# Kernel optimization log

Measured on AMD Instinct MI355X. Metric: run time of the kernel, lower is better.

Reference implementation:

```python
import jax, jax.numpy as jnp
import numpy as np

B, D, K, C, A = 131072, 300, 32, 384, 18  # batch, emb dim, num_negs, codebook size, attr dims


def setup_inputs() -> dict:
    key = jax.random.key(0)
    ks = jax.random.split(key, 12)
    x = jax.random.normal(ks[0], (B, D), dtype=jnp.float32)
    # codebook of all possible attribute one-hot combinations (binary rows)
    codebook = (jax.random.uniform(ks[1], (C, A)) < 0.5).astype(jnp.float32)
    tgt = jax.random.randint(ks[2], (B,), 0, C)
    y = codebook[tgt]                                   # true labels are codebook rows
    ob = (jax.random.uniform(ks[3], (B, A)) > 0.1).astype(jnp.float32)  # observed-attr mask
    neg_idx = jax.random.randint(ks[4], (B, K), 0, C)   # negative sample indices
    s = 0.05
    W1 = jax.random.normal(ks[5], (D, 64), dtype=jnp.float32) * s
    b1 = jnp.zeros((64,), jnp.float32)
    W2 = jax.random.normal(ks[6], (64, 32), dtype=jnp.float32) * s
    b2 = jnp.zeros((32,), jnp.float32)
    W3 = jax.random.normal(ks[7], (32, A), dtype=jnp.float32) * s
    b3 = jnp.zeros((A,), jnp.float32)
    return dict(x=x, y=y, ob=ob, codebook=codebook, W1=W1, b1=b1, W2=W2, b2=b2,
                W3=W3, b3=b3, neg_idx=neg_idx)


def reference(x, y, ob, codebook, W1, b1, W2, b2, W3, b3, neg_idx):
    # MLP: Linear->Sigmoid->Linear->Sigmoid->Linear
    h = jax.nn.sigmoid(x @ W1 + b1)
    h = jax.nn.sigmoid(h @ W2 + b2)
    W_user = h @ W3 + b3                                # [B, A]
    W_compact = W_user * ob                             # [B, A]
    # rows kept by the original index_select: nonzero row-sum -> mask instead
    mask = (jnp.sum(W_compact, axis=1) != 0).astype(W_compact.dtype)  # [B]
    neg = codebook[neg_idx]                             # [B, K, A] gather
    # neg log term: sum over negatives and attr dims of log sigmoid(-(neg * w))
    neg_log = jax.nn.log_sigmoid(-neg * W_compact[:, None, :]).sum(axis=(1, 2))  # [B]
    pos_log = jax.nn.log_sigmoid(W_compact * y).sum(axis=1)                      # [B]
    cnt = jnp.maximum(jnp.sum(mask), 1.0)
    loss = -jnp.sum(mask * (pos_log + neg_log)) / cnt
    return W_user, loss
```

## Files before the change

### kernel.cpp

```cpp
#include <hip/hip_runtime.h>

typedef short bf16x8 __attribute__((ext_vector_type(8)));
typedef unsigned short u16;
typedef u16 u16x4 __attribute__((ext_vector_type(4)));
typedef float f32x4 __attribute__((ext_vector_type(4)));

constexpr int TPB  = 256;
constexpr int RPB  = 64;
constexpr int DIM  = 300;
constexpr int KPAD = 320;
constexpr int NKT  = 10;
constexpr int H1N  = 64;
constexpr int H2N  = 32;
constexpr int NA   = 18;
constexpr int NK   = 32;
constexpr int NC   = 384;
constexpr float LOG_HALF = -0.6931471805599453f;

__device__ __forceinline__ float fast_sigmoid(float z) {
    return __builtin_amdgcn_rcpf(1.0f + __expf(-z));
}
__device__ __forceinline__ float lsig(float z) {
    return fminf(z, 0.0f) - __logf(1.0f + __expf(-fabsf(z)));
}
__device__ __forceinline__ u16 f2bf(float f) {
    unsigned u = __builtin_bit_cast(unsigned, f);
    return (u16)((u + 0x7FFFu + ((u >> 16) & 1u)) >> 16);
}
__device__ __forceinline__ unsigned spread8(unsigned v) {
    v = (v | (v << 12)) & 0x000F000Fu;
    v = (v | (v << 6))  & 0x03030303u;
    v = (v | (v << 3))  & 0x11111111u;
    return v;
}

__global__ __launch_bounds__(384)
void prep_k(const float* __restrict__ W1, const float* __restrict__ W2,
            const float* __restrict__ W3, const float* __restrict__ cbf,
            u16* __restrict__ w1t, u16* __restrict__ w2t, u16* __restrict__ w3t,
            unsigned* __restrict__ cbw)
{
    const int c = blockIdx.x;
    const int t = threadIdx.x;
    if (c < 64) {
        if (t < KPAD)
            w1t[c * KPAD + t] = f2bf((t < DIM) ? W1[t * H1N + c] : 0.0f);
    } else if (c == 64) {
        if (t < NC) {
            unsigned bits = 0u;
            #pragma unroll
            for (int a = 0; a < NA; ++a)
                bits |= (cbf[t * NA + a] != 0.0f) ? (1u << a) : 0u;
            cbw[t] = bits;
        }
    } else if (c == 65) {
        for (int e = t; e < H2N * H1N; e += 384) {
            const int n = e >> 6, k = e & 63;
            w2t[e] = f2bf(W2[k * H2N + n]);
        }
    } else {
        for (int e = t; e < H2N * H2N; e += 384) {
            const int n = e >> 5, k = e & 31;
            w3t[e] = f2bf((n < NA) ? W3[k * NA + n] : 0.0f);
        }
    }
}

__global__ __launch_bounds__(TPB, 4)
void fused_mf2(const float* __restrict__ x, const float* __restrict__ y,
               const float* __restrict__ ob, const float* __restrict__ b1,
               const float* __restrict__ b2, const float* __restrict__ b3,
               const int* __restrict__ neg_idx,
               const u16* __restrict__ w1t, const u16* __restrict__ w2t,
               const u16* __restrict__ w3t, const unsigned* __restrict__ cbw,
               float* __restrict__ out_wu, float2* __restrict__ blk_part)
{
    __shared__ __align__(16) unsigned char smem[40960];
    u16*      xs      = (u16*)smem;
    u16*      h1s     = (u16*)smem;
    u16*      h2s     = (u16*)(smem + 8192);
    float*    wus     = (float*)(smem + 12288);
    unsigned* cb_bits = (unsigned*)(smem + 17408);
    float*    wsum    = (float*)(smem + 18944);
    int*      wcnt    = (int*)(smem + 18960);

    const int tid  = threadIdx.x;
    const int lane = tid & 63;
    const int wv   = tid >> 6;
    const int l15  = lane & 15;
    const int kg   = (lane >> 4) * 8;
    const long brow = (long)blockIdx.x * RPB;
    const float* xg = x + brow * DIM;

    float4 va[7], vb[6], vc[6];
    #pragma unroll
    for (int ch = 0; ch < 7; ++ch)
        va[ch] = *(const float4*)(xg + (long)(ch * TPB + tid) * 4);
    #pragma unroll
    for (int ch = 0; ch < 6; ++ch)
        vb[ch] = *(const float4*)(xg + (long)((7 + ch) * TPB + tid) * 4);
    __builtin_amdgcn_sched_barrier(0);
    #pragma unroll
    for (int ch = 0; ch < 7; ++ch) {
        const int f = ch * TPB + tid;
        const int row = f / 75, k = (f - row * 75) * 4;
        const int kk = k ^ ((row & 7) << 3);
        u16x4 pk = { f2bf(va[ch].x), f2bf(va[ch].y), f2bf(va[ch].z), f2bf(va[ch].w) };
        *(u16x4*)(xs + row * KPAD + kk) = pk;
    }
    __builtin_amdgcn_sched_barrier(0);
    #pragma unroll
    for (int ch = 0; ch < 6; ++ch) {
        const int f = (13 + ch) * TPB + tid;
        vc[ch] = (ch < 5 || f < 4800) ? *(const float4*)(xg + (long)f * 4)
                                      : make_float4(0.f, 0.f, 0.f, 0.f);
    }
    __builtin_amdgcn_sched_barrier(0);
    #pragma unroll
    for (int ch = 0; ch < 6; ++ch) {
        const int f = (7 + ch) * TPB + tid;
        const int row = f / 75, k = (f - row * 75) * 4;
        const int kk = k ^ ((row & 7) << 3);
        u16x4 pk = { f2bf(vb[ch].x), f2bf(vb[ch].y), f2bf(vb[ch].z), f2bf(vb[ch].w) };
        *(u16x4*)(xs + row * KPAD + kk) = pk;
    }
    #pragma unroll
    for (int ch = 0; ch < 6; ++ch) {
        const int f = (13 + ch) * TPB + tid;
        if (ch < 5 || f < 4800) {
            const int row = f / 75, k = (f - row * 75) * 4;
            const int kk = k ^ ((row & 7) << 3);
            u16x4 pk = { f2bf(vc[ch].x), f2bf(vc[ch].y), f2bf(vc[ch].z), f2bf(vc[ch].w) };
            *(u16x4*)(xs + row * KPAD + kk) = pk;
        }
    }
    #pragma unroll
    for (int uu = 0; uu < 5; ++uu) {
        const int e = uu * TPB + tid;
        const int row = e / 20, kp = e - row * 20;
        xs[row * KPAD + ((DIM + kp) ^ ((row & 7) << 3))] = 0;
    }

    const int colB = wv * 16 + l15;
    bf16x8 bfr[NKT];
    #pragma unroll
    for (int kt = 0; kt < NKT; ++kt)
        bfr[kt] = *(const bf16x8*)(w1t + colB * KPAD + kt * 32 + kg);
    const unsigned cbv0 = cbw[tid];
    const unsigned cbv1 = (tid < NC - TPB) ? cbw[tid + TPB] : 0u;

    __syncthreads();

    f32x4 acc[4];
    #pragma unroll
    for (int rt = 0; rt < 4; ++rt) acc[rt] = (f32x4){0.f, 0.f, 0.f, 0.f};
    #pragma unroll
    for (int kt = 0; kt < NKT; ++kt) {
        bf16x8 afr[4];
        #pragma unroll
        for (int rt = 0; rt < 4; ++rt) {
            const int row = rt * 16 + l15;
            afr[rt] = *(const bf16x8*)(xs + ((row * KPAD + kt * 32 + kg) ^ ((row & 7) << 3)));
        }
        #pragma unroll
        for (int rt = 0; rt < 4; ++rt)
            acc[rt] = __builtin_amdgcn_mfma_f32_16x16x32_bf16(afr[rt], bfr[kt], acc[rt], 0, 0, 0);
    }
    __syncthreads();

    const float b1v = b1[colB];
    #pragma unroll
    for (int rt = 0; rt < 4; ++rt) {
        #pragma unroll
        for (int j = 0; j < 4; ++j) {
            const int row = rt * 16 + (lane >> 4) * 4 + j;
            h1s[(row * H1N + colB) ^ ((row & 7) << 3)] = f2bf(fast_sigmoid(acc[rt][j] + b1v));
        }
    }
    cb_bits[tid] = cbv0;
    if (tid < NC - TPB) cb_bits[tid + TPB] = cbv1;

    const int rloc = wv * 16 + (lane >> 2);
    const int p    = lane & 3;
    const long bds = brow + rloc;
    const int4* nbp = (const int4*)(neg_idx + bds * NK + p * 8);
    const int4 n0 = nbp[0], n1 = nbp[1];
    const float* obr = ob + bds * NA + p * 4;
    const float2 oA = *(const float2*)obr, oB = *(const float2*)(obr + 2);
    const float  oT = (p < 2) ? ob[bds * NA + 16 + p] : 0.f;
    const float* yr = y + bds * NA + p * 4;
    const float2 yA = *(const float2*)yr, yB = *(const float2*)(yr + 2);
    const float  yT = (p < 2) ? y[bds * NA + 16 + p] : 0.f;

    __syncthreads();

    const int rowA = wv * 16 + l15;
    bf16x8 a2[2];
    #pragma unroll
    for (int kt = 0; kt < 2; ++kt)
        a2[kt] = *(const bf16x8*)(h1s + ((rowA * H1N + kt * 32 + kg) ^ ((rowA & 7) << 3)));
    f32x4 acc2[2];
    #pragma unroll
    for (int ct = 0; ct < 2; ++ct) {
        const float bb = b2[ct * 16 + l15];
        acc2[ct] = (f32x4){bb, bb, bb, bb};
    }
    #pragma unroll
    for (int ct = 0; ct < 2; ++ct)
        #pragma unroll
        for (int kt = 0; kt < 2; ++kt) {
            const bf16x8 bfr2 = *(const bf16x8*)(w2t + (ct * 16 + l15) * H1N + kt * 32 + kg);
            acc2[ct] = __builtin_amdgcn_mfma_f32_16x16x32_bf16(a2[kt], bfr2, acc2[ct], 0, 0, 0);
        }
    #pragma unroll
    for (int ct = 0; ct < 2; ++ct) {
        #pragma unroll
        for (int j = 0; j < 4; ++j) {
            const int row = wv * 16 + (lane >> 4) * 4 + j;
            const int col = ct * 16 + l15;
            h2s[(row * H2N + col) ^ ((row & 3) << 3)] = f2bf(fast_sigmoid(acc2[ct][j]));
        }
    }

    const bf16x8 a3 = *(const bf16x8*)(h2s + ((rowA * H2N + kg) ^ ((rowA & 3) << 3)));
    f32x4 acc3[2];
    #pragma unroll
    for (int ct = 0; ct < 2; ++ct) {
        const int col = ct * 16 + l15;
        const float bb = (col < NA) ? b3[col] : 0.f;
        acc3[ct] = (f32x4){bb, bb, bb, bb};
    }
    #pragma unroll
    for (int ct = 0; ct < 2; ++ct) {
        const bf16x8 bfr3 = *(const bf16x8*)(w3t + (ct * 16 + l15) * H2N + kg);
        acc3[ct] = __builtin_amdgcn_mfma_f32_16x16x32_bf16(a3, bfr3, acc3[ct], 0, 0, 0);
    }
    #pragma unroll
    for (int j = 0; j < 4; ++j) {
        const int row = wv * 16 + (lane >> 4) * 4 + j;
        wus[row * 20 + l15] = acc3[0][j];
        if (l15 < 2) wus[row * 20 + 16 + l15] = acc3[1][j];
    }
    __builtin_amdgcn_sched_barrier(0);

    const float4 wA = *(const float4*)(wus + rloc * 20 + p * 4);
    const float  wT = (p < 2) ? wus[rloc * 20 + 16 + p] : 0.f;

    const float wcv[4] = {wA.x * oA.x, wA.y * oA.y, wA.z * oB.x, wA.w * oB.y};
    const float yvv[4] = {yA.x, yA.y, yB.x, yB.y};
    const float wcT = wT * oT;
    float ssum = wcv[0] + wcv[1] + wcv[2] + wcv[3] + wcT;
    ssum += __shfl_xor(ssum, 1);
    ssum += __shfl_xor(ssum, 2);
    const int mask = (ssum != 0.0f) ? 1 : 0;

    const int ids[8] = {n0.x, n0.y, n0.z, n0.w, n1.x, n1.y, n1.z, n1.w};
    unsigned c0 = 0u, c1 = 0u, c2 = 0u;
    #pragma unroll
    for (int kk = 0; kk < 8; ++kk) {
        const unsigned bits = cb_bits[ids[kk]];
        c0 += spread8(bits & 0xFFu);
        c1 += spread8((bits >> 8) & 0xFFu);
        const unsigned t = (bits >> 16) & 3u;
        c2 += (t | (t << 3)) & 0x11u;
    }
    unsigned e0 = c0 & 0x0F0F0F0Fu;
    unsigned e1 = (c0 >> 4) & 0x0F0F0F0Fu;
    unsigned e2 = c1 & 0x0F0F0F0Fu;
    unsigned e3 = (c1 >> 4) & 0x0F0F0F0Fu;
    unsigned e4 = (c2 & 15u) | (((c2 >> 4) & 15u) << 8);
    e0 += __shfl_xor((int)e0, 1); e0 += __shfl_xor((int)e0, 2);
    e1 += __shfl_xor((int)e1, 1); e1 += __shfl_xor((int)e1, 2);
    e2 += __shfl_xor((int)e2, 1); e2 += __shfl_xor((int)e2, 2);
    e3 += __shfl_xor((int)e3, 1); e3 += __shfl_xor((int)e3, 2);
    e4 += __shfl_xor((int)e4, 1); e4 += __shfl_xor((int)e4, 2);

    float rsum = 0.0f;
    #pragma unroll
    for (int i = 0; i < 4; ++i) {
        const unsigned regE = ((i & 1) == 0) ? ((p < 2) ? e0 : e2)
                                             : ((p < 2) ? e1 : e3);
        const int sh = (((p & 1) * 2) + (i >> 1)) * 8;
        const int cn = (int)((regE >> sh) & 0xFFu);
        const float w = wcv[i];
        const float pos = (yvv[i] != 0.0f) ? lsig(w) : LOG_HALF;
        rsum += pos + (float)cn * lsig(-w) + (float)(NK - cn) * LOG_HALF;
    }
    if (p < 2) {
        const int cn = (int)((e4 >> (p * 8)) & 0xFFu);
        const float pos = (yT != 0.0f) ? lsig(wcT) : LOG_HALF;
        rsum += pos + (float)cn * lsig(-wcT) + (float)(NK - cn) * LOG_HALF;
    }
    rsum += __shfl_xor(rsum, 1);
    rsum += __shfl_xor(rsum, 2);

    float vv = (p == 0 && mask) ? rsum : 0.0f;
    int   mm = (p == 0) ? mask : 0;
    #pragma unroll
    for (int off = 32; off > 0; off >>= 1) {
        vv += __shfl_down(vv, off);
        mm += __shfl_down(mm, off);
    }
    if (lane == 0) { wsum[wv] = vv; wcnt[wv] = mm; }
    __syncthreads();

    float* og = out_wu + brow * NA;
    #pragma unroll
    for (int g = tid; g < RPB * NA; g += TPB) {
        const int row = g / NA, col = g - row * NA;
        og[g] = wus[row * 20 + col];
    }
    if (tid == 0) {
        const float s = wsum[0] + wsum[1] + wsum[2] + wsum[3];
        const int   c = wcnt[0] + wcnt[1] + wcnt[2] + wcnt[3];
        blk_part[blockIdx.x] = make_float2(s, (float)c);
    }
}

__global__ void finalize_k(const float2* __restrict__ part, int nblk,
                           float* __restrict__ out_loss) {
    __shared__ float ss[4], sc[4];
    float s = 0.f, c = 0.f;
    for (int i = threadIdx.x; i < nblk; i += 256) {
        const float2 v = part[i];
        s += v.x; c += v.y;
    }
    #pragma unroll
    for (int off = 32; off > 0; off >>= 1) {
        s += __shfl_down(s, off);
        c += __shfl_down(c, off);
    }
    const int wv = threadIdx.x >> 6;
    if ((threadIdx.x & 63) == 0) { ss[wv] = s; sc[wv] = c; }
    __syncthreads();
    if (threadIdx.x == 0) {
        const float S = ss[0] + ss[1] + ss[2] + ss[3];
        const float C = sc[0] + sc[1] + sc[2] + sc[3];
        out_loss[0] = -S / fmaxf(C, 1.0f);
    }
}

extern "C" void kernel_launch(void* const* d_in, const int* in_sizes, int n_in,
                              void* d_out, int out_size, void* d_ws, size_t ws_size,
                              hipStream_t stream)
{
    const float* x   = (const float*)d_in[0];
    const float* y   = (const float*)d_in[1];
    const float* ob  = (const float*)d_in[2];
    const float* cb  = (const float*)d_in[3];
    const float* W1  = (const float*)d_in[4];
    const float* b1  = (const float*)d_in[5];
    const float* W2  = (const float*)d_in[6];
    const float* b2  = (const float*)d_in[7];
    const float* W3  = (const float*)d_in[8];
    const float* b3  = (const float*)d_in[9];
    const int*   neg = (const int*)d_in[10];

    const int B = in_sizes[0] / DIM;
    const int nblk = B / RPB;

    float*    out_wu = (float*)d_out;
    u16*      w1t  = (u16*)d_ws;
    u16*      w2t  = (u16*)((char*)d_ws + 40960);
    u16*      w3t  = (u16*)((char*)d_ws + 45056);
    unsigned* cbw  = (unsigned*)((char*)d_ws + 47104);
    float2*   part = (float2*)((char*)d_ws + 48640);

    prep_k<<<67, 384, 0, stream>>>(W1, W2, W3, cb, w1t, w2t, w3t, cbw);
    fused_mf2<<<nblk, TPB, 0, stream>>>(x, y, ob, b1, b2, b3,
                                        neg, w1t, w2t, w3t, cbw, out_wu, part);
    finalize_k<<<1, TPB, 0, stream>>>(part, nblk, out_wu + (long)B * NA);
}
```

Before: 51.86 us.

## Double block to 512 threads, splitting MLP rows/columns across eight waves

Raises the fused kernel's block size from 256 to 512 threads with 64 rows per block. Layer-1 work is split into two row halves times four column quarters, and layers 2 and 3 are split by output column tile, so each wave holds fewer accumulators and fewer x loads in flight. The loss stage runs only on the first four waves. The aim is more waves per CU and lower per-thread register pressure, at the cost of an extra block barrier and idle waves during the loss stage.

```diff
diff --git a/kernel.cpp b/kernel.cpp
--- a/kernel.cpp
+++ b/kernel.cpp
@@ -5,7 +5,8 @@
 typedef u16 u16x4 __attribute__((ext_vector_type(4)));
 typedef float f32x4 __attribute__((ext_vector_type(4)));
 
-constexpr int TPB  = 256;
+constexpr int TPB  = 512;
+constexpr int FTPB = 256;
 constexpr int RPB  = 64;
 constexpr int DIM  = 300;
 constexpr int KPAD = 320;
@@ -66,7 +67,7 @@
     }
 }
 
-__global__ __launch_bounds__(TPB, 4)
+__global__ __launch_bounds__(TPB, 6)
 void fused_mf2(const float* __restrict__ x, const float* __restrict__ y,
                const float* __restrict__ ob, const float* __restrict__ b1,
                const float* __restrict__ b2, const float* __restrict__ b3,
@@ -89,19 +90,21 @@
     const int wv   = tid >> 6;
     const int l15  = lane & 15;
     const int kg   = (lane >> 4) * 8;
+    const int rh   = wv >> 2;
+    const int cq   = wv & 3;
     const long brow = (long)blockIdx.x * RPB;
     const float* xg = x + brow * DIM;
 
-    float4 va[7], vb[6], vc[6];
-    #pragma unroll
-    for (int ch = 0; ch < 7; ++ch)
+    float4 va[4], vb[3], vc[3];
+    #pragma unroll
+    for (int ch = 0; ch < 4; ++ch)
         va[ch] = *(const float4*)(xg + (long)(ch * TPB + tid) * 4);
     #pragma unroll
-    for (int ch = 0; ch < 6; ++ch)
-        vb[ch] = *(const float4*)(xg + (long)((7 + ch) * TPB + tid) * 4);
+    for (int ch = 0; ch < 3; ++ch)
+        vb[ch] = *(const float4*)(xg + (long)((4 + ch) * TPB + tid) * 4);
     __builtin_amdgcn_sched_barrier(0);
     #pragma unroll
-    for (int ch = 0; ch < 7; ++ch) {
+    for (int ch = 0; ch < 4; ++ch) {
         const int f = ch * TPB + tid;
         const int row = f / 75, k = (f - row * 75) * 4;
         const int kk = k ^ ((row & 7) << 3);
@@ -110,24 +113,24 @@
     }
     __builtin_amdgcn_sched_barrier(0);
     #pragma unroll
-    for (int ch = 0; ch < 6; ++ch) {
-        const int f = (13 + ch) * TPB + tid;
-        vc[ch] = (ch < 5 || f < 4800) ? *(const float4*)(xg + (long)f * 4)
+    for (int ch = 0; ch < 3; ++ch) {
+        const int f = (7 + ch) * TPB + tid;
+        vc[ch] = (ch < 2 || f < 4800) ? *(const float4*)(xg + (long)f * 4)
                                       : make_float4(0.f, 0.f, 0.f, 0.f);
     }
     __builtin_amdgcn_sched_barrier(0);
     #pragma unroll
-    for (int ch = 0; ch < 6; ++ch) {
-        const int f = (7 + ch) * TPB + tid;
+    for (int ch = 0; ch < 3; ++ch) {
+        const int f = (4 + ch) * TPB + tid;
         const int row = f / 75, k = (f - row * 75) * 4;
         const int kk = k ^ ((row & 7) << 3);
         u16x4 pk = { f2bf(vb[ch].x), f2bf(vb[ch].y), f2bf(vb[ch].z), f2bf(vb[ch].w) };
         *(u16x4*)(xs + row * KPAD + kk) = pk;
     }
     #pragma unroll
-    for (int ch = 0; ch < 6; ++ch) {
-        const int f = (13 + ch) * TPB + tid;
-        if (ch < 5 || f < 4800) {
+    for (int ch = 0; ch < 3; ++ch) {
+        const int f = (7 + ch) * TPB + tid;
+        if (ch < 2 || f < 4800) {
             const int row = f / 75, k = (f - row * 75) * 4;
             const int kk = k ^ ((row & 7) << 3);
             u16x4 pk = { f2bf(vc[ch].x), f2bf(vc[ch].y), f2bf(vc[ch].z), f2bf(vc[ch].w) };
@@ -135,177 +138,170 @@
         }
     }
     #pragma unroll
-    for (int uu = 0; uu < 5; ++uu) {
+    for (int uu = 0; uu < 3; ++uu) {
         const int e = uu * TPB + tid;
-        const int row = e / 20, kp = e - row * 20;
-        xs[row * KPAD + ((DIM + kp) ^ ((row & 7) << 3))] = 0;
-    }
-
-    const int colB = wv * 16 + l15;
+        if (uu < 2 || tid < 256) {
+            const int row = e / 20, kp = e - row * 20;
+            xs[row * KPAD + ((DIM + kp) ^ ((row & 7) << 3))] = 0;
+        }
+    }
+
+    const int colB = cq * 16 + l15;
     bf16x8 bfr[NKT];
     #pragma unroll
     for (int kt = 0; kt < NKT; ++kt)
         bfr[kt] = *(const bf16x8*)(w1t + colB * KPAD + kt * 32 + kg);
-    const unsigned cbv0 = cbw[tid];
-    const unsigned cbv1 = (tid < NC - TPB) ? cbw[tid + TPB] : 0u;
-
-    __syncthreads();
-
-    f32x4 acc[4];
-    #pragma unroll
-    for (int rt = 0; rt < 4; ++rt) acc[rt] = (f32x4){0.f, 0.f, 0.f, 0.f};
+    const unsigned cbv0 = (tid < NC) ? cbw[tid] : 0u;
+
+    __syncthreads();
+
+    f32x4 acc[2];
+    #pragma unroll
+    for (int rt = 0; rt < 2; ++rt) acc[rt] = (f32x4){0.f, 0.f, 0.f, 0.f};
     #pragma unroll
     for (int kt = 0; kt < NKT; ++kt) {
-        bf16x8 afr[4];
-        #pragma unroll
-        for (int rt = 0; rt < 4; ++rt) {
-            const int row = rt * 16 + l15;
+        bf16x8 afr[2];
+        #pragma unroll
+        for (int rt = 0; rt < 2; ++rt) {
+            const int row = rh * 32 + rt * 16 + l15;
             afr[rt] = *(const bf16x8*)(xs + ((row * KPAD + kt * 32 + kg) ^ ((row & 7) << 3)));
         }
         #pragma unroll
-        for (int rt = 0; rt < 4; ++rt)
+        for (int rt = 0; rt < 2; ++rt)
             acc[rt] = __builtin_amdgcn_mfma_f32_16x16x32_bf16(afr[rt], bfr[kt], acc[rt], 0, 0, 0);
     }
     __syncthreads();
 
     const float b1v = b1[colB];
     #pragma unroll
-    for (int rt = 0; rt < 4; ++rt) {
+    for (int rt = 0; rt < 2; ++rt) {
         #pragma unroll
         for (int j = 0; j < 4; ++j) {
-            const int row = rt * 16 + (lane >> 4) * 4 + j;
+            const int row = rh * 32 + rt * 16 + (lane >> 4) * 4 + j;
             h1s[(row * H1N + colB) ^ ((row & 7) << 3)] = f2bf(fast_sigmoid(acc[rt][j] + b1v));
         }
     }
-    cb_bits[tid] = cbv0;
-    if (tid < NC - TPB) cb_bits[tid + TPB] = cbv1;
-
-    const int rloc = wv * 16 + (lane >> 2);
+    if (tid < NC) cb_bits[tid] = cbv0;
+
+    const int rloc = (wv & 3) * 16 + (lane >> 2);
     const int p    = lane & 3;
     const long bds = brow + rloc;
-    const int4* nbp = (const int4*)(neg_idx + bds * NK + p * 8);
-    const int4 n0 = nbp[0], n1 = nbp[1];
-    const float* obr = ob + bds * NA + p * 4;
-    const float2 oA = *(const float2*)obr, oB = *(const float2*)(obr + 2);
-    const float  oT = (p < 2) ? ob[bds * NA + 16 + p] : 0.f;
-    const float* yr = y + bds * NA + p * 4;
-    const float2 yA = *(const float2*)yr, yB = *(const float2*)(yr + 2);
-    const float  yT = (p < 2) ? y[bds * NA + 16 + p] : 0.f;
-
-    __syncthreads();
-
-    const int rowA = wv * 16 + l15;
+    int4 n0 = make_int4(0, 0, 0, 0), n1 = make_int4(0, 0, 0, 0);
+    float2 oA = make_float2(0.f, 0.f), oB = oA, yA = oA, yB = oA;
+    float oT = 0.f, yT = 0.f;
+    if (wv < 4) {
+        const int4* nbp = (const int4*)(neg_idx + bds * NK + p * 8);
+        n0 = nbp[0]; n1 = nbp[1];
+        const float* obr = ob + bds * NA + p * 4;
+        oA = *(const float2*)obr; oB = *(const float2*)(obr + 2);
+        if (p < 2) oT = ob[bds * NA + 16 + p];
+        const float* yr = y + bds * NA + p * 4;
+        yA = *(const float2*)yr; yB = *(const float2*)(yr + 2);
+        if (p < 2) yT = y[bds * NA + 16 + p];
+    }
+
+    __syncthreads();
+
+    const int rowA = (wv & 3) * 16 + l15;
+    const int ct2  = wv >> 2;
+    const int colC = ct2 * 16 + l15;
     bf16x8 a2[2];
     #pragma unroll
     for (int kt = 0; kt < 2; ++kt)
         a2[kt] = *(const bf16x8*)(h1s + ((rowA * H1N + kt * 32 + kg) ^ ((rowA & 7) << 3)));
-    f32x4 acc2[2];
-    #pragma unroll
-    for (int ct = 0; ct < 2; ++ct) {
-        const float bb = b2[ct * 16 + l15];
-        acc2[ct] = (f32x4){bb, bb, bb, bb};
-    }
-    #pragma unroll
-    for (int ct = 0; ct < 2; ++ct)
-        #pragma unroll
-        for (int kt = 0; kt < 2; ++kt) {
-            const bf16x8 bfr2 = *(const bf16x8*)(w2t + (ct * 16 + l15) * H1N + kt * 32 + kg);
-            acc2[ct] = __builtin_amdgcn_mfma_f32_16x16x32_bf16(a2[kt], bfr2, acc2[ct], 0, 0, 0);
-        }
-    #pragma unroll
-    for (int ct = 0; ct < 2; ++ct) {
-        #pragma unroll
-        for (int j = 0; j < 4; ++j) {
-            const int row = wv * 16 + (lane >> 4) * 4 + j;
-            const int col = ct * 16 + l15;
-            h2s[(row * H2N + col) ^ ((row & 3) << 3)] = f2bf(fast_sigmoid(acc2[ct][j]));
-        }
-    }
+    const float bb2 = b2[colC];
+    f32x4 acc2 = (f32x4){bb2, bb2, bb2, bb2};
+    #pragma unroll
+    for (int kt = 0; kt < 2; ++kt) {
+        const bf16x8 bfr2 = *(const bf16x8*)(w2t + colC * H1N + kt * 32 + kg);
+        acc2 = __builtin_amdgcn_mfma_f32_16x16x32_bf16(a2[kt], bfr2, acc2, 0, 0, 0);
+    }
+    #pragma unroll
+    for (int j = 0; j < 4; ++j) {
+        const int row = (wv & 3) * 16 + (lane >> 4) * 4 + j;
+        h2s[(row * H2N + colC) ^ ((row & 3) << 3)] = f2bf(fast_sigmoid(acc2[j]));
+    }
+    __syncthreads();
 
     const bf16x8 a3 = *(const bf16x8*)(h2s + ((rowA * H2N + kg) ^ ((rowA & 3) << 3)));
-    f32x4 acc3[2];
-    #pragma unroll
-    for (int ct = 0; ct < 2; ++ct) {
-        const int col = ct * 16 + l15;
-        const float bb = (col < NA) ? b3[col] : 0.f;
-        acc3[ct] = (f32x4){bb, bb, bb, bb};
-    }
-    #pragma unroll
-    for (int ct = 0; ct < 2; ++ct) {
-        const bf16x8 bfr3 = *(const bf16x8*)(w3t + (ct * 16 + l15) * H2N + kg);
-        acc3[ct] = __builtin_amdgcn_mfma_f32_16x16x32_bf16(a3, bfr3, acc3[ct], 0, 0, 0);
+    const float bb3 = (colC < NA) ? b3[colC] : 0.f;
+    f32x4 acc3 = (f32x4){bb3, bb3, bb3, bb3};
+    {
+        const bf16x8 bfr3 = *(const bf16x8*)(w3t + colC * H2N + kg);
+        acc3 = __builtin_amdgcn_mfma_f32_16x16x32_bf16(a3, bfr3, acc3, 0, 0, 0);
     }
     #pragma unroll
     for (int j = 0; j < 4; ++j) {
-        const int row = wv * 16 + (lane >> 4) * 4 + j;
-        wus[row * 20 + l15] = acc3[0][j];
-        if (l15 < 2) wus[row * 20 + 16 + l15] = acc3[1][j];
-    }
-    __builtin_amdgcn_sched_barrier(0);
-
-    const float4 wA = *(const float4*)(wus + rloc * 20 + p * 4);
-    const float  wT = (p < 2) ? wus[rloc * 20 + 16 + p] : 0.f;
-
-    const float wcv[4] = {wA.x * oA.x, wA.y * oA.y, wA.z * oB.x, wA.w * oB.y};
-    const float yvv[4] = {yA.x, yA.y, yB.x, yB.y};
-    const float wcT = wT * oT;
-    float ssum = wcv[0] + wcv[1] + wcv[2] + wcv[3] + wcT;
-    ssum += __shfl_xor(ssum, 1);
-    ssum += __shfl_xor(ssum, 2);
-    const int mask = (ssum != 0.0f) ? 1 : 0;
-
-    const int ids[8] = {n0.x, n0.y, n0.z, n0.w, n1.x, n1.y, n1.z, n1.w};
-    unsigned c0 = 0u, c1 = 0u, c2 = 0u;
-    #pragma unroll
-    for (int kk = 0; kk < 8; ++kk) {
-        const unsigned bits = cb_bits[ids[kk]];
-        c0 += spread8(bits & 0xFFu);
-        c1 += spread8((bits >> 8) & 0xFFu);
-        const unsigned t = (bits >> 16) & 3u;
-        c2 += (t | (t << 3)) & 0x11u;
-    }
-    unsigned e0 = c0 & 0x0F0F0F0Fu;
-    unsigned e1 = (c0 >> 4) & 0x0F0F0F0Fu;
-    unsigned e2 = c1 & 0x0F0F0F0Fu;
-    unsigned e3 = (c1 >> 4) & 0x0F0F0F0Fu;
-    unsigned e4 = (c2 & 15u) | (((c2 >> 4) & 15u) << 8);
-    e0 += __shfl_xor((int)e0, 1); e0 += __shfl_xor((int)e0, 2);
-    e1 += __shfl_xor((int)e1, 1); e1 += __shfl_xor((int)e1, 2);
-    e2 += __shfl_xor((int)e2, 1); e2 += __shfl_xor((int)e2, 2);
-    e3 += __shfl_xor((int)e3, 1); e3 += __shfl_xor((int)e3, 2);
-    e4 += __shfl_xor((int)e4, 1); e4 += __shfl_xor((int)e4, 2);
-
-    float rsum = 0.0f;
-    #pragma unroll
-    for (int i = 0; i < 4; ++i) {
-        const unsigned regE = ((i & 1) == 0) ? ((p < 2) ? e0 : e2)
-                                             : ((p < 2) ? e1 : e3);
-        const int sh = (((p & 1) * 2) + (i >> 1)) * 8;
-        const int cn = (int)((regE >> sh) & 0xFFu);
-        const float w = wcv[i];
-        const float pos = (yvv[i] != 0.0f) ? lsig(w) : LOG_HALF;
-        rsum += pos + (float)cn * lsig(-w) + (float)(NK - cn) * LOG_HALF;
-    }
-    if (p < 2) {
-        const int cn = (int)((e4 >> (p * 8)) & 0xFFu);
-        const float pos = (yT != 0.0f) ? lsig(wcT) : LOG_HALF;
-        rsum += pos + (float)cn * lsig(-wcT) + (float)(NK - cn) * LOG_HALF;
-    }
-    rsum += __shfl_xor(rsum, 1);
-    rsum += __shfl_xor(rsum, 2);
-
-    float vv = (p == 0 && mask) ? rsum : 0.0f;
-    int   mm = (p == 0) ? mask : 0;
-    #pragma unroll
-    for (int off = 32; off > 0; off >>= 1) {
-        vv += __shfl_down(vv, off);
-        mm += __shfl_down(mm, off);
-    }
-    if (lane == 0) { wsum[wv] = vv; wcnt[wv] = mm; }
+        const int row = (wv & 3) * 16 + (lane >> 4) * 4 + j;
+        if (ct2 == 0)          wus[row * 20 + l15] = acc3[j];
+        else if (l15 < 2)      wus[row * 20 + 16 + l15] = acc3[j];
+    }
+    __syncthreads();
+
+    if (wv < 4) {
+        const float4 wA = *(const float4*)(wus + rloc * 20 + p * 4);
+        const float  wT = (p < 2) ? wus[rloc * 20 + 16 + p] : 0.f;
+
+        const float wcv[4] = {wA.x * oA.x, wA.y * oA.y, wA.z * oB.x, wA.w * oB.y};
+        const float yvv[4] = {yA.x, yA.y, yB.x, yB.y};
+        const float wcT = wT * oT;
+        float ssum = wcv[0] + wcv[1] + wcv[2] + wcv[3] + wcT;
+        ssum += __shfl_xor(ssum, 1);
+        ssum += __shfl_xor(ssum, 2);
+        const int mask = (ssum != 0.0f) ? 1 : 0;
+
+        const int ids[8] = {n0.x, n0.y, n0.z, n0.w, n1.x, n1.y, n1.z, n1.w};
+        unsigned c0 = 0u, c1 = 0u, c2 = 0u;
+        #pragma unroll
+        for (int kk = 0; kk < 8; ++kk) {
+            const unsigned bits = cb_bits[ids[kk]];
+            c0 += spread8(bits & 0xFFu);
+            c1 += spread8((bits >> 8) & 0xFFu);
+            const unsigned t = (bits >> 16) & 3u;
+            c2 += (t | (t << 3)) & 0x11u;
+        }
+        unsigned e0 = c0 & 0x0F0F0F0Fu;
+        unsigned e1 = (c0 >> 4) & 0x0F0F0F0Fu;
+        unsigned e2 = c1 & 0x0F0F0F0Fu;
+        unsigned e3 = (c1 >> 4) & 0x0F0F0F0Fu;
+        unsigned e4 = (c2 & 15u) | (((c2 >> 4) & 15u) << 8);
+        e0 += __shfl_xor((int)e0, 1); e0 += __shfl_xor((int)e0, 2);
+        e1 += __shfl_xor((int)e1, 1); e1 += __shfl_xor((int)e1, 2);
+        e2 += __shfl_xor((int)e2, 1); e2 += __shfl_xor((int)e2, 2);
+        e3 += __shfl_xor((int)e3, 1); e3 += __shfl_xor((int)e3, 2);
+        e4 += __shfl_xor((int)e4, 1); e4 += __shfl_xor((int)e4, 2);
+
+        float rsum = 0.0f;
+        #pragma unroll
+        for (int i = 0; i < 4; ++i) {
+            const unsigned regE = ((i & 1) == 0) ? ((p < 2) ? e0 : e2)
+                                                 : ((p < 2) ? e1 : e3);
+            const int sh = (((p & 1) * 2) + (i >> 1)) * 8;
+            const int cn = (int)((regE >> sh) & 0xFFu);
+            const float w = wcv[i];
+            const float pos = (yvv[i] != 0.0f) ? lsig(w) : LOG_HALF;
+            rsum += pos + (float)cn * lsig(-w) + (float)(NK - cn) * LOG_HALF;
+        }
+        if (p < 2) {
+            const int cn = (int)((e4 >> (p * 8)) & 0xFFu);
+            const float pos = (yT != 0.0f) ? lsig(wcT) : LOG_HALF;
+            rsum += pos + (float)cn * lsig(-wcT) + (float)(NK - cn) * LOG_HALF;
+        }
+        rsum += __shfl_xor(rsum, 1);
+        rsum += __shfl_xor(rsum, 2);
+
+        float vv = (p == 0 && mask) ? rsum : 0.0f;
+        int   mm = (p == 0) ? mask : 0;
+        #pragma unroll
+        for (int off = 32; off > 0; off >>= 1) {
+            vv += __shfl_down(vv, off);
+            mm += __shfl_down(mm, off);
+        }
+        if (lane == 0) { wsum[wv] = vv; wcnt[wv] = mm; }
+    }
     __syncthreads();
 
     float* og = out_wu + brow * NA;
-    #pragma unroll
     for (int g = tid; g < RPB * NA; g += TPB) {
         const int row = g / NA, col = g - row * NA;
         og[g] = wus[row * 20 + col];
@@ -317,11 +313,12 @@
     }
 }
 
-__global__ void finalize_k(const float2* __restrict__ part, int nblk,
-                           float* __restrict__ out_loss) {
-    __shared__ float ss[4], sc[4];
+__global__ __launch_bounds__(FTPB)
+void finalize_k(const float2* __restrict__ part, int nblk,
+                float* __restrict__ out_loss) {
+    __shared__ float ss[FTPB / 64], sc[FTPB / 64];
     float s = 0.f, c = 0.f;
-    for (int i = threadIdx.x; i < nblk; i += 256) {
+    for (int i = threadIdx.x; i < nblk; i += FTPB) {
         const float2 v = part[i];
         s += v.x; c += v.y;
     }
@@ -334,8 +331,9 @@
     if ((threadIdx.x & 63) == 0) { ss[wv] = s; sc[wv] = c; }
     __syncthreads();
     if (threadIdx.x == 0) {
-        const float S = ss[0] + ss[1] + ss[2] + ss[3];
-        const float C = sc[0] + sc[1] + sc[2] + sc[3];
+        float S = 0.f, C = 0.f;
+        #pragma unroll
+        for (int w = 0; w < FTPB / 64; ++w) { S += ss[w]; C += sc[w]; }
         out_loss[0] = -S / fmaxf(C, 1.0f);
     }
 }
@@ -369,5 +367,5 @@
     prep_k<<<67, 384, 0, stream>>>(W1, W2, W3, cb, w1t, w2t, w3t, cbw);
     fused_mf2<<<nblk, TPB, 0, stream>>>(x, y, ob, b1, b2, b3,
                                         neg, w1t, w2t, w3t, cbw, out_wu, part);
-    finalize_k<<<1, TPB, 0, stream>>>(part, nblk, out_wu + (long)B * NA);
-}
+    finalize_k<<<1, FTPB, 0, stream>>>(part, nblk, out_wu + (long)B * NA);
+}
```

Result: slower. 58.75 us (+13.3%).
